# Optimization experiments

Hardware: AMD Instinct MI355X
Metric: run time of the kernel (lower is better)

Reference implementation:

```python
import jax, jax.numpy as jnp
import numpy as np

N_NODES = 100000
N_EDGES = 1280000
D_IN = 64
D_HID = 128
D_OUT = 64


def sage_conv(x, src, dst, W_l, b_l, W_r, n_nodes):
    # PyG SAGEConv (aggr='mean', root_weight=True):
    #   out_i = W_l @ mean_{j in N(i)} x_j + b_l + W_r @ x_i
    msg = x[src]  # [E, d] gather of source-node features
    agg = jax.ops.segment_sum(msg, dst, num_segments=n_nodes)  # [N, d]
    cnt = jax.ops.segment_sum(jnp.ones((src.shape[0], 1), x.dtype), dst,
                              num_segments=n_nodes)  # [N, 1]
    mean = agg / jnp.maximum(cnt, 1.0)  # zero-neighbor nodes -> 0 (matches scatter-mean)
    return mean @ W_l.T + b_l + x @ W_r.T


def setup_inputs() -> dict:
    key = jax.random.key(0)
    ks = jax.random.split(key, 8)
    x = jax.random.normal(ks[0], (N_NODES, D_IN), dtype=jnp.float32)
    edge_index = jax.random.randint(ks[1], (2, N_EDGES), 0, N_NODES, dtype=jnp.int64)
    s = 0.05
    W_l1 = jax.random.normal(ks[2], (D_HID, D_IN), dtype=jnp.float32) * s
    b_l1 = jnp.zeros((D_HID,), dtype=jnp.float32)
    W_r1 = jax.random.normal(ks[3], (D_HID, D_IN), dtype=jnp.float32) * s
    W_l2 = jax.random.normal(ks[4], (D_OUT, D_HID), dtype=jnp.float32) * s
    b_l2 = jnp.zeros((D_OUT,), dtype=jnp.float32)
    W_r2 = jax.random.normal(ks[5], (D_OUT, D_HID), dtype=jnp.float32) * s
    return {"x": x, "edge_index": edge_index,
            "W_l1": W_l1, "b_l1": b_l1, "W_r1": W_r1,
            "W_l2": W_l2, "b_l2": b_l2, "W_r2": W_r2}


def reference(x, edge_index, W_l1, b_l1, W_r1, W_l2, b_l2, W_r2):
    src, dst = edge_index[0], edge_index[1]
    n = x.shape[0]
    h = sage_conv(x, src, dst, W_l1, b_l1, W_r1, n)
    h = jax.nn.relu(h)
    out = sage_conv(h, src, dst, W_l2, b_l2, W_r2, n)
    return out
```

## Files before the change

### kernel.cpp

```cpp
#include <hip/hip_runtime.h>
#include <cstdint>
#include <cstddef>

typedef __attribute__((ext_vector_type(8))) short short8;
typedef __attribute__((ext_vector_type(4))) float floatx4;
typedef __attribute__((ext_vector_type(2))) float floatx2;
typedef __attribute__((ext_vector_type(4))) int intx4;

static constexpr int DIN  = 64;
static constexpr int DHID = 128;
static constexpr int BSH  = 7;
static constexpr int BNODES = 1 << BSH;
static constexpr int TILE = 8192;
static constexpr int CAP  = 4096;
static constexpr unsigned SENT = 0xFFFFFFFFu;

__device__ inline short f2bf(float f) {
  unsigned u = __float_as_uint(f);
  u += 0x7FFF + ((u >> 16) & 1);
  return (short)(u >> 16);
}
__device__ inline float bf2f(short s) {
  return __uint_as_float(((unsigned)(unsigned short)s) << 16);
}
__device__ inline floatx2 bfpair(unsigned u) {
  floatx2 r;
  r[0] = __uint_as_float(u << 16);
  r[1] = __uint_as_float(u & 0xFFFF0000u);
  return r;
}

__global__ __launch_bounds__(256) void part_prep_kernel(const void* edges, long long nmax,
    int* __restrict__ bucket_cursor, int* __restrict__ real_cnt,
    unsigned* __restrict__ packed, int E, int NB,
    const float* __restrict__ x,
    const float* __restrict__ Wl1, const float* __restrict__ Wr1,
    const float* __restrict__ Wl2, const float* __restrict__ Wr2,
    short* __restrict__ xb, short* __restrict__ wc1, short* __restrict__ wc2,
    int nx, int gP, int gx)
{
  __shared__ unsigned sval[TILE];
  __shared__ unsigned saux[TILE];
  __shared__ int hist[1024];
  __shared__ int gb[1024];
  __shared__ int smode;
  int t = threadIdx.x;
  int blk = blockIdx.x;
  if (blk >= gP) {
    int b = blk - gP;
    if (b < gx) {
      int i0 = (b * 256 + t) * 8;
      if (i0 < nx) {
        floatx4 f0 = *(const floatx4*)&x[i0];
        floatx4 f1 = *(const floatx4*)&x[i0 + 4];
        short8 o;
        o[0]=f2bf(f0[0]); o[1]=f2bf(f0[1]); o[2]=f2bf(f0[2]); o[3]=f2bf(f0[3]);
        o[4]=f2bf(f1[0]); o[5]=f2bf(f1[1]); o[6]=f2bf(f1[2]); o[7]=f2bf(f1[3]);
        *(short8*)&xb[i0] = o;
      }
    } else {
      int wb = b - gx;
      int idx = ((wb & 15) * 256 + t) * 4;
      int n = idx >> 7, k = idx & 127;
      const float* src;
      if (wb < 16) src = (k < 64) ? &Wl1[n * 64 + k] : &Wr1[n * 64 + (k - 64)];
      else         src = (n < 64) ? &Wl2[n * 128 + k] : &Wr2[(n - 64) * 128 + k];
      floatx4 f = *(const floatx4*)src;
      short* dst = (wb < 16 ? wc1 : wc2) + idx;
      dst[0]=f2bf(f[0]); dst[1]=f2bf(f[1]); dst[2]=f2bf(f[2]); dst[3]=f2bf(f[3]);
    }
    return;
  }
  int base = blk * TILE;
  int cnt_here = E - base; if (cnt_here > TILE) cnt_here = TILE;
  for (int i = t; i < NB; i += 256) hist[i] = 0;
  if (t == 0) smode = 1;
  __syncthreads();
  {
    const long long* e64 = (const long long*)edges;
    int nchk = E < 256 ? E : 256;
    bool ok = true;
    for (int i = t; i < nchk; i += 256) {
      long long v = e64[i];
      if (v < 0 || v >= nmax) ok = false;
    }
    if (!ok) smode = 0;
  }
  __syncthreads();
  bool m64 = (smode != 0);
  #pragma unroll 4
  for (int c = 0; c < TILE / 256; ++c) {
    int idx = c * 256 + t;
    if (idx < cnt_here) {
      int i = base + idx;
      int s, d;
      if (m64) { const long long* e = (const long long*)edges; s = (int)e[i]; d = (int)e[(size_t)E + i]; }
      else     { const int*       e = (const int*)edges;       s = e[i];      d = e[(size_t)E + i]; }
      int b = d >> BSH;
      int rank = atomicAdd(&hist[b], 1);
      sval[idx] = ((unsigned)(d & (BNODES - 1)) << 17) | (unsigned)s;
      saux[idx] = ((unsigned)b << 13) | (unsigned)rank;
    }
  }
  __syncthreads();
  for (int b = t; b < NB; b += 256) {
    int cnt = hist[b];
    int gbase = 0;
    if (cnt > 0) {
      int pad = (cnt + 15) & ~15;
      gbase = b * CAP + atomicAdd(&bucket_cursor[b], pad);
      atomicAdd(&real_cnt[b], cnt);
      for (int j = cnt; j < pad; ++j) packed[gbase + j] = SENT;
    }
    gb[b] = gbase;
  }
  __syncthreads();
  #pragma unroll 4
  for (int c = 0; c < TILE / 256; ++c) {
    int idx = c * 256 + t;
    if (idx < cnt_here) {
      unsigned a = saux[idx];
      packed[gb[a >> 13] + (a & 0x1FFFu)] = sval[idx];
    }
  }
}

__global__ __launch_bounds__(256) void bucket_sort_kernel(const unsigned* __restrict__ packed,
                                                          const int* __restrict__ bucket_cursor,
                                                          const int* __restrict__ real_cnt,
                                                          int* __restrict__ row_ptr,
                                                          int* __restrict__ sorted_src, int N, int E) {
  __shared__ int nhist[BNODES];
  __shared__ int cur[BNODES];
  __shared__ int wsum[4];
  __shared__ int redsum[4];
  int b = blockIdx.x, t = threadIdx.x;
  int partial = 0;
  for (int i = t; i < b; i += 256) partial += real_cnt[i];
  #pragma unroll
  for (int off = 1; off < 64; off <<= 1) partial += __shfl_xor(partial, off, 64);
  if ((t & 63) == 0) redsum[t >> 6] = partial;
  if (t < BNODES) nhist[t] = 0;
  if (b == 0 && t == 0) row_ptr[N] = E;
  __syncthreads();
  int eb = redsum[0] + redsum[1] + redsum[2] + redsum[3];
  int n0 = b << BSH;
  int nn = N - n0; if (nn > BNODES) nn = BNODES;
  int rbeg = b * CAP, rcnt = bucket_cursor[b];
  for (int i = t; i < rcnt; i += 256) {
    unsigned p = packed[rbeg + i];
    if (p != SENT) atomicAdd(&nhist[p >> 17], 1);
  }
  __syncthreads();
  int lane = t & 63, w = t >> 6;
  int v = (t < BNODES) ? nhist[t] : 0;
  int val = v;
  #pragma unroll
  for (int off = 1; off < 64; off <<= 1) {
    int u = __shfl_up(val, off, 64);
    if (lane >= off) val += u;
  }
  if (lane == 63) wsum[w] = val;
  __syncthreads();
  int pre = (w == 1) ? wsum[0] : 0;
  int excl = pre + val - v;
  if (t < nn) { row_ptr[n0 + t] = eb + excl; cur[t] = eb + excl; }
  __syncthreads();
  for (int i = t; i < rcnt; i += 256) {
    unsigned p = packed[rbeg + i];
    if (p != SENT) {
      int pos = atomicAdd(&cur[p >> 17], 1);
      sorted_src[pos] = (int)(p & 0x1FFFFu);
    }
  }
}

template <bool EPI>
__global__ __launch_bounds__(256) void agg_bf16_kernel(const short* __restrict__ feat,
                                                       const int* __restrict__ row_ptr,
                                                       const int* __restrict__ srcs,
                                                       const float* __restrict__ rbuf,
                                                       const float* __restrict__ bias,
                                                       short* __restrict__ outb,
                                                       float* __restrict__ outf, int N) {
  int node = blockIdx.x * 32 + (threadIdx.x >> 3);
  if (node >= N) return;
  int c = threadIdx.x & 7;
  const short* fbase = feat + c * 8;
  int beg = row_ptr[node], end = row_ptr[node + 1];
  floatx2 acc2[4];
  #pragma unroll
  for (int k = 0; k < 4; ++k) acc2[k] = (floatx2){0.f, 0.f};
  int e = beg;
  for (; e + 8 <= end; e += 8) {
    intx4 sa = *(const intx4*)&srcs[e];
    intx4 sb = *(const intx4*)&srcs[e + 4];
    short8 v0 = *(const short8*)&fbase[(size_t)sa[0] * 64];
    short8 v1 = *(const short8*)&fbase[(size_t)sa[1] * 64];
    short8 v2 = *(const short8*)&fbase[(size_t)sa[2] * 64];
    short8 v3 = *(const short8*)&fbase[(size_t)sa[3] * 64];
    short8 v4 = *(const short8*)&fbase[(size_t)sb[0] * 64];
    short8 v5 = *(const short8*)&fbase[(size_t)sb[1] * 64];
    short8 v6 = *(const short8*)&fbase[(size_t)sb[2] * 64];
    short8 v7 = *(const short8*)&fbase[(size_t)sb[3] * 64];
    const unsigned* u0 = (const unsigned*)&v0;
    const unsigned* u1 = (const unsigned*)&v1;
    const unsigned* u2 = (const unsigned*)&v2;
    const unsigned* u3 = (const unsigned*)&v3;
    const unsigned* u4 = (const unsigned*)&v4;
    const unsigned* u5 = (const unsigned*)&v5;
    const unsigned* u6 = (const unsigned*)&v6;
    const unsigned* u7 = (const unsigned*)&v7;
    #pragma unroll
    for (int k = 0; k < 4; ++k) {
      floatx2 s01 = bfpair(u0[k]) + bfpair(u1[k]);
      floatx2 s23 = bfpair(u2[k]) + bfpair(u3[k]);
      floatx2 s45 = bfpair(u4[k]) + bfpair(u5[k]);
      floatx2 s67 = bfpair(u6[k]) + bfpair(u7[k]);
      acc2[k] += (s01 + s23) + (s45 + s67);
    }
  }
  for (; e + 4 <= end; e += 4) {
    intx4 sa = *(const intx4*)&srcs[e];
    short8 v0 = *(const short8*)&fbase[(size_t)sa[0] * 64];
    short8 v1 = *(const short8*)&fbase[(size_t)sa[1] * 64];
    short8 v2 = *(const short8*)&fbase[(size_t)sa[2] * 64];
    short8 v3 = *(const short8*)&fbase[(size_t)sa[3] * 64];
    const unsigned* u0 = (const unsigned*)&v0;
    const unsigned* u1 = (const unsigned*)&v1;
    const unsigned* u2 = (const unsigned*)&v2;
    const unsigned* u3 = (const unsigned*)&v3;
    #pragma unroll
    for (int k = 0; k < 4; ++k) {
      floatx2 s01 = bfpair(u0[k]) + bfpair(u1[k]);
      floatx2 s23 = bfpair(u2[k]) + bfpair(u3[k]);
      acc2[k] += s01 + s23;
    }
  }
  for (; e < end; ++e) {
    short8 v = *(const short8*)&fbase[(size_t)srcs[e] * 64];
    const unsigned* u = (const unsigned*)&v;
    #pragma unroll
    for (int k = 0; k < 4; ++k) acc2[k] += bfpair(u[k]);
  }
  float acc[8];
  #pragma unroll
  for (int k = 0; k < 4; ++k) { acc[2 * k] = acc2[k][0]; acc[2 * k + 1] = acc2[k][1]; }
  float inv = 1.f / fmaxf((float)(end - beg), 1.f);
  if (!EPI) {
    short8 o;
    #pragma unroll
    for (int j = 0; j < 8; ++j) o[j] = f2bf(acc[j] * inv);
    *(short8*)&outb[(size_t)node * 64 + c * 8] = o;
  } else {
    floatx4 b0 = *(const floatx4*)&bias[c * 8];
    floatx4 b1 = *(const floatx4*)&bias[c * 8 + 4];
    floatx4 r0 = *(const floatx4*)&rbuf[(size_t)node * 64 + c * 8];
    floatx4 r1 = *(const floatx4*)&rbuf[(size_t)node * 64 + c * 8 + 4];
    floatx4 o0, o1;
    #pragma unroll
    for (int j = 0; j < 4; ++j) {
      o0[j] = acc[j] * inv + b0[j] + r0[j];
      o1[j] = acc[4 + j] * inv + b1[j] + r1[j];
    }
    *(floatx4*)&outf[(size_t)node * 64 + c * 8]     = o0;
    *(floatx4*)&outf[(size_t)node * 64 + c * 8 + 4] = o1;
  }
}

__global__ __launch_bounds__(256) void fused_gemm_kernel(
    const short* __restrict__ Aa, const short* __restrict__ Ab,
    const short* __restrict__ wc1, const short* __restrict__ wc2,
    const float* __restrict__ bias1,
    short* __restrict__ Cg, float* __restrict__ Cr, int M)
{
  __shared__ short Ws[128][136];
  __shared__ short Hs[64][136];
  int t = threadIdx.x;
  #pragma unroll
  for (int i = 0; i < 8; ++i) {
    int idx = i * 256 + t;
    int r = idx >> 4, c8 = (idx & 15) * 8;
    *(short8*)&Ws[r][c8] = *(const short8*)&wc1[r * 128 + c8];
  }
  __syncthreads();
  int wv = t >> 6, lane = t & 63, q = lane >> 4, l15 = lane & 15;
  int m0 = blockIdx.x * 64 + wv * 16;
  int row = m0 + l15;
  bool rowok = row < M;
  floatx4 acc[8];
  #pragma unroll
  for (int nt = 0; nt < 8; ++nt) acc[nt] = (floatx4){0.f, 0.f, 0.f, 0.f};
  #pragma unroll
  for (int ko = 0; ko < 4; ++ko) {
    const short* Asrc = (ko < 2) ? Aa : Ab;
    short8 a = {0, 0, 0, 0, 0, 0, 0, 0};
    if (rowok) a = *(const short8*)&Asrc[(size_t)row * 64 + (ko & 1) * 32 + q * 8];
    #pragma unroll
    for (int nt = 0; nt < 8; ++nt) {
      short8 b = *(const short8*)&Ws[nt * 16 + l15][ko * 32 + q * 8];
      acc[nt] = __builtin_amdgcn_mfma_f32_16x16x32_bf16(a, b, acc[nt], 0, 0, 0);
    }
  }
  #pragma unroll
  for (int nt = 0; nt < 8; ++nt) {
    int n = nt * 16 + l15;
    float bv = bias1[n];
    #pragma unroll
    for (int r2 = 0; r2 < 4; ++r2) {
      int lr = wv * 16 + q * 4 + r2;
      float v = fmaxf(acc[nt][r2] + bv, 0.f);
      Hs[lr][n] = f2bf(v);
    }
  }
  __syncthreads();
  #pragma unroll
  for (int i = 0; i < 8; ++i) {
    int idx = i * 256 + t;
    int r = idx >> 4, c8 = (idx & 15) * 8;
    *(short8*)&Ws[r][c8] = *(const short8*)&wc2[r * 128 + c8];
  }
  __syncthreads();
  #pragma unroll
  for (int nt = 0; nt < 8; ++nt) acc[nt] = (floatx4){0.f, 0.f, 0.f, 0.f};
  #pragma unroll
  for (int ko = 0; ko < 4; ++ko) {
    short8 a = *(const short8*)&Hs[wv * 16 + l15][ko * 32 + q * 8];
    #pragma unroll
    for (int nt = 0; nt < 8; ++nt) {
      short8 b = *(const short8*)&Ws[nt * 16 + l15][ko * 32 + q * 8];
      acc[nt] = __builtin_amdgcn_mfma_f32_16x16x32_bf16(a, b, acc[nt], 0, 0, 0);
    }
  }
  #pragma unroll
  for (int nt = 0; nt < 8; ++nt) {
    int n = nt * 16 + l15;
    #pragma unroll
    for (int r2 = 0; r2 < 4; ++r2) {
      int mr = m0 + q * 4 + r2;
      if (mr >= M) continue;
      float v = acc[nt][r2];
      if (nt < 4) Cg[(size_t)mr * 64 + n] = f2bf(v);
      else        Cr[(size_t)mr * 64 + (n - 64)] = v;
    }
  }
}

extern "C" void kernel_launch(void* const* d_in, const int* in_sizes, int n_in,
                              void* d_out, int out_size, void* d_ws, size_t ws_size,
                              hipStream_t stream) {
  const float* x   = (const float*)d_in[0];
  const void*  ei  = d_in[1];
  const float* Wl1 = (const float*)d_in[2];
  const float* bl1 = (const float*)d_in[3];
  const float* Wr1 = (const float*)d_in[4];
  const float* Wl2 = (const float*)d_in[5];
  const float* bl2 = (const float*)d_in[6];
  const float* Wr2 = (const float*)d_in[7];
  int N = in_sizes[0] / DIN;
  int E = in_sizes[1] / 2;
  int NB = (N + BNODES - 1) / BNODES;

  char* w = (char*)d_ws;
  size_t off = 0;
  auto alloc = [&](size_t bytes) -> void* {
    void* p = w + off;
    off += (bytes + 255) & ~(size_t)255;
    return p;
  };
  int*      bcur       = (int*)alloc((size_t)NB * 8);
  int*      rcnt       = bcur + NB;
  int*      row_ptr    = (int*)alloc(((size_t)N + 1) * 4);
  unsigned* packed     = (unsigned*)alloc((size_t)NB * CAP * 4);
  int*      sorted_src = (int*)alloc((size_t)E * 4);
  short*    xb         = (short*)alloc((size_t)N * 64 * 2);
  short*    meanb      = (short*)alloc((size_t)N * 64 * 2);
  float*    rbuf       = (float*)alloc((size_t)N * 64 * 4);
  short*    wc1        = (short*)alloc(128 * 128 * 2);
  short*    wc2        = (short*)alloc(128 * 128 * 2);
  (void)ws_size; (void)n_in; (void)out_size;

  hipMemsetAsync(bcur, 0, (size_t)NB * 8, stream);

  int nx = N * DIN;
  int gx = (nx / 8 + 255) / 256;
  int gP = (E + TILE - 1) / TILE;
  part_prep_kernel<<<gP + gx + 32, 256, 0, stream>>>(ei, (long long)N, bcur, rcnt, packed,
                                                     E, NB, x, Wl1, Wr1, Wl2, Wr2,
                                                     xb, wc1, wc2, nx, gP, gx);

  bucket_sort_kernel<<<NB, 256, 0, stream>>>(packed, bcur, rcnt, row_ptr, sorted_src, N, E);

  int gN32 = (N + 31) / 32;
  agg_bf16_kernel<false><<<gN32, 256, 0, stream>>>(xb, row_ptr, sorted_src, nullptr, nullptr, meanb, nullptr, N);

  int gm = (N + 63) / 64;
  fused_gemm_kernel<<<gm, 256, 0, stream>>>(meanb, xb, wc1, wc2, bl1, meanb, rbuf, N);

  agg_bf16_kernel<true><<<gN32, 256, 0, stream>>>(meanb, row_ptr, sorted_src, rbuf, bl2, nullptr, (float*)d_out, N);
}
```

Baseline: 203.5 us.

## Replace two-level bucket sort with global-atomic CSR build; widen GEMM tile to 128 rows

Replaces the LDS-partitioned bucket sort (partition kernel plus per-bucket sort kernel) with a classic counting sort: a global atomic degree histogram, a single-block 1024-thread scan, and a scatter pass that uses global atomics on per-node cursors. Separately, the fused GEMM now processes 128 rows per block, with two M-subtiles per wave sharing each B fragment, to improve weight reuse. The new CSR path depends on contended global atomics and on a single-workgroup serial scan over 100k nodes, and it gives up the locality of the bucketed scatter, so it may be slower. The GEMM change doubles accumulator registers and LDS use.

```diff
diff --git a/kernel.cpp b/kernel.cpp
--- a/kernel.cpp
+++ b/kernel.cpp
@@ -9,11 +9,7 @@
 
 static constexpr int DIN  = 64;
 static constexpr int DHID = 128;
-static constexpr int BSH  = 7;
-static constexpr int BNODES = 1 << BSH;
-static constexpr int TILE = 8192;
-static constexpr int CAP  = 4096;
-static constexpr unsigned SENT = 0xFFFFFFFFu;
+static constexpr int HTILE = 2048;
 
 __device__ inline short f2bf(float f) {
   unsigned u = __float_as_uint(f);
@@ -30,24 +26,19 @@
   return r;
 }
 
-__global__ __launch_bounds__(256) void part_prep_kernel(const void* edges, long long nmax,
-    int* __restrict__ bucket_cursor, int* __restrict__ real_cnt,
-    unsigned* __restrict__ packed, int E, int NB,
+__global__ __launch_bounds__(256) void prep_hist_kernel(const void* edges, long long nmax,
+    int* __restrict__ deg, int E,
     const float* __restrict__ x,
     const float* __restrict__ Wl1, const float* __restrict__ Wr1,
     const float* __restrict__ Wl2, const float* __restrict__ Wr2,
     short* __restrict__ xb, short* __restrict__ wc1, short* __restrict__ wc2,
-    int nx, int gP, int gx)
+    int nx, int gH, int gx)
 {
-  __shared__ unsigned sval[TILE];
-  __shared__ unsigned saux[TILE];
-  __shared__ int hist[1024];
-  __shared__ int gb[1024];
   __shared__ int smode;
   int t = threadIdx.x;
   int blk = blockIdx.x;
-  if (blk >= gP) {
-    int b = blk - gP;
+  if (blk >= gH) {
+    int b = blk - gH;
     if (b < gx) {
       int i0 = (b * 256 + t) * 8;
       if (i0 < nx) {
@@ -71,9 +62,6 @@
     }
     return;
   }
-  int base = blk * TILE;
-  int cnt_here = E - base; if (cnt_here > TILE) cnt_here = TILE;
-  for (int i = t; i < NB; i += 256) hist[i] = 0;
   if (t == 0) smode = 1;
   __syncthreads();
   {
@@ -88,89 +76,82 @@
   }
   __syncthreads();
   bool m64 = (smode != 0);
-  #pragma unroll 4
-  for (int c = 0; c < TILE / 256; ++c) {
+  int base = blk * HTILE;
+  int cnt_here = E - base; if (cnt_here > HTILE) cnt_here = HTILE;
+  #pragma unroll
+  for (int c = 0; c < HTILE / 256; ++c) {
+    int idx = c * 256 + t;
+    if (idx < cnt_here) {
+      int i = base + idx;
+      int d;
+      if (m64) { const long long* e = (const long long*)edges; d = (int)e[(size_t)E + i]; }
+      else     { const int*       e = (const int*)edges;       d = e[(size_t)E + i]; }
+      atomicAdd(&deg[d], 1);
+    }
+  }
+}
+
+__global__ __launch_bounds__(1024) void scan_kernel(const int* __restrict__ deg,
+                                                    int* __restrict__ row_ptr,
+                                                    int* __restrict__ cur, int N, int E) {
+  __shared__ int wsums[16];
+  int t = threadIdx.x;
+  int per = (N + 1023) / 1024;
+  int i0 = t * per;
+  int i1 = i0 + per; if (i1 > N) i1 = N;
+  int s = 0;
+  for (int i = i0; i < i1; ++i) s += deg[i];
+  int lane = t & 63, w = t >> 6;
+  int val = s;
+  #pragma unroll
+  for (int off = 1; off < 64; off <<= 1) {
+    int u = __shfl_up(val, off, 64);
+    if (lane >= off) val += u;
+  }
+  if (lane == 63) wsums[w] = val;
+  __syncthreads();
+  int wpre = 0;
+  for (int ww = 0; ww < w; ++ww) wpre += wsums[ww];
+  int run = wpre + val - s;
+  for (int i = i0; i < i1; ++i) {
+    row_ptr[i] = run;
+    cur[i] = run;
+    run += deg[i];
+  }
+  if (t == 0) row_ptr[N] = E;
+}
+
+__global__ __launch_bounds__(256) void scatter_kernel(const void* edges, long long nmax,
+                                                      int* __restrict__ cur,
+                                                      int* __restrict__ sorted_src, int E) {
+  __shared__ int smode;
+  int t = threadIdx.x;
+  if (t == 0) smode = 1;
+  __syncthreads();
+  {
+    const long long* e64 = (const long long*)edges;
+    int nchk = E < 256 ? E : 256;
+    bool ok = true;
+    for (int i = t; i < nchk; i += 256) {
+      long long v = e64[i];
+      if (v < 0 || v >= nmax) ok = false;
+    }
+    if (!ok) smode = 0;
+  }
+  __syncthreads();
+  bool m64 = (smode != 0);
+  int base = blockIdx.x * HTILE;
+  int cnt_here = E - base; if (cnt_here > HTILE) cnt_here = HTILE;
+  #pragma unroll
+  for (int c = 0; c < HTILE / 256; ++c) {
     int idx = c * 256 + t;
     if (idx < cnt_here) {
       int i = base + idx;
       int s, d;
       if (m64) { const long long* e = (const long long*)edges; s = (int)e[i]; d = (int)e[(size_t)E + i]; }
       else     { const int*       e = (const int*)edges;       s = e[i];      d = e[(size_t)E + i]; }
-      int b = d >> BSH;
-      int rank = atomicAdd(&hist[b], 1);
-      sval[idx] = ((unsigned)(d & (BNODES - 1)) << 17) | (unsigned)s;
-      saux[idx] = ((unsigned)b << 13) | (unsigned)rank;
-    }
-  }
-  __syncthreads();
-  for (int b = t; b < NB; b += 256) {
-    int cnt = hist[b];
-    int gbase = 0;
-    if (cnt > 0) {
-      int pad = (cnt + 15) & ~15;
-      gbase = b * CAP + atomicAdd(&bucket_cursor[b], pad);
-      atomicAdd(&real_cnt[b], cnt);
-      for (int j = cnt; j < pad; ++j) packed[gbase + j] = SENT;
-    }
-    gb[b] = gbase;
-  }
-  __syncthreads();
-  #pragma unroll 4
-  for (int c = 0; c < TILE / 256; ++c) {
-    int idx = c * 256 + t;
-    if (idx < cnt_here) {
-      unsigned a = saux[idx];
-      packed[gb[a >> 13] + (a & 0x1FFFu)] = sval[idx];
-    }
-  }
-}
-
-__global__ __launch_bounds__(256) void bucket_sort_kernel(const unsigned* __restrict__ packed,
-                                                          const int* __restrict__ bucket_cursor,
-                                                          const int* __restrict__ real_cnt,
-                                                          int* __restrict__ row_ptr,
-                                                          int* __restrict__ sorted_src, int N, int E) {
-  __shared__ int nhist[BNODES];
-  __shared__ int cur[BNODES];
-  __shared__ int wsum[4];
-  __shared__ int redsum[4];
-  int b = blockIdx.x, t = threadIdx.x;
-  int partial = 0;
-  for (int i = t; i < b; i += 256) partial += real_cnt[i];
-  #pragma unroll
-  for (int off = 1; off < 64; off <<= 1) partial += __shfl_xor(partial, off, 64);
-  if ((t & 63) == 0) redsum[t >> 6] = partial;
-  if (t < BNODES) nhist[t] = 0;
-  if (b == 0 && t == 0) row_ptr[N] = E;
-  __syncthreads();
-  int eb = redsum[0] + redsum[1] + redsum[2] + redsum[3];
-  int n0 = b << BSH;
-  int nn = N - n0; if (nn > BNODES) nn = BNODES;
-  int rbeg = b * CAP, rcnt = bucket_cursor[b];
-  for (int i = t; i < rcnt; i += 256) {
-    unsigned p = packed[rbeg + i];
-    if (p != SENT) atomicAdd(&nhist[p >> 17], 1);
-  }
-  __syncthreads();
-  int lane = t & 63, w = t >> 6;
-  int v = (t < BNODES) ? nhist[t] : 0;
-  int val = v;
-  #pragma unroll
-  for (int off = 1; off < 64; off <<= 1) {
-    int u = __shfl_up(val, off, 64);
-    if (lane >= off) val += u;
-  }
-  if (lane == 63) wsum[w] = val;
-  __syncthreads();
-  int pre = (w == 1) ? wsum[0] : 0;
-  int excl = pre + val - v;
-  if (t < nn) { row_ptr[n0 + t] = eb + excl; cur[t] = eb + excl; }
-  __syncthreads();
-  for (int i = t; i < rcnt; i += 256) {
-    unsigned p = packed[rbeg + i];
-    if (p != SENT) {
-      int pos = atomicAdd(&cur[p >> 17], 1);
-      sorted_src[pos] = (int)(p & 0x1FFFFu);
+      int pos = atomicAdd(&cur[d], 1);
+      sorted_src[pos] = s;
     }
   }
 }
@@ -275,7 +256,7 @@
     short* __restrict__ Cg, float* __restrict__ Cr, int M)
 {
   __shared__ short Ws[128][136];
-  __shared__ short Hs[64][136];
+  __shared__ short Hs[128][136];
   int t = threadIdx.x;
   #pragma unroll
   for (int i = 0; i < 8; ++i) {
@@ -285,32 +266,41 @@
   }
   __syncthreads();
   int wv = t >> 6, lane = t & 63, q = lane >> 4, l15 = lane & 15;
-  int m0 = blockIdx.x * 64 + wv * 16;
-  int row = m0 + l15;
-  bool rowok = row < M;
-  floatx4 acc[8];
-  #pragma unroll
-  for (int nt = 0; nt < 8; ++nt) acc[nt] = (floatx4){0.f, 0.f, 0.f, 0.f};
+  int m0 = blockIdx.x * 128 + wv * 32;
+  floatx4 acc[2][8];
+  #pragma unroll
+  for (int mt = 0; mt < 2; ++mt)
+    #pragma unroll
+    for (int nt = 0; nt < 8; ++nt) acc[mt][nt] = (floatx4){0.f, 0.f, 0.f, 0.f};
   #pragma unroll
   for (int ko = 0; ko < 4; ++ko) {
     const short* Asrc = (ko < 2) ? Aa : Ab;
-    short8 a = {0, 0, 0, 0, 0, 0, 0, 0};
-    if (rowok) a = *(const short8*)&Asrc[(size_t)row * 64 + (ko & 1) * 32 + q * 8];
+    short8 a[2];
+    #pragma unroll
+    for (int mt = 0; mt < 2; ++mt) {
+      int row = m0 + mt * 16 + l15;
+      a[mt] = (short8){0, 0, 0, 0, 0, 0, 0, 0};
+      if (row < M) a[mt] = *(const short8*)&Asrc[(size_t)row * 64 + (ko & 1) * 32 + q * 8];
+    }
     #pragma unroll
     for (int nt = 0; nt < 8; ++nt) {
-      short8 b = *(const short8*)&Ws[nt * 16 + l15][ko * 32 + q * 8];
-      acc[nt] = __builtin_amdgcn_mfma_f32_16x16x32_bf16(a, b, acc[nt], 0, 0, 0);
-    }
-  }
-  #pragma unroll
-  for (int nt = 0; nt < 8; ++nt) {
-    int n = nt * 16 + l15;
-    float bv = bias1[n];
-    #pragma unroll
-    for (int r2 = 0; r2 < 4; ++r2) {
-      int lr = wv * 16 + q * 4 + r2;
-      float v = fmaxf(acc[nt][r2] + bv, 0.f);
-      Hs[lr][n] = f2bf(v);
+      short8 bfr = *(const short8*)&Ws[nt * 16 + l15][ko * 32 + q * 8];
+      acc[0][nt] = __builtin_amdgcn_mfma_f32_16x16x32_bf16(a[0], bfr, acc[0][nt], 0, 0, 0);
+      acc[1][nt] = __builtin_amdgcn_mfma_f32_16x16x32_bf16(a[1], bfr, acc[1][nt], 0, 0, 0);
+    }
+  }
+  #pragma unroll
+  for (int mt = 0; mt < 2; ++mt) {
+    #pragma unroll
+    for (int nt = 0; nt < 8; ++nt) {
+      int n = nt * 16 + l15;
+      float bv = bias1[n];
+      #pragma unroll
+      for (int r2 = 0; r2 < 4; ++r2) {
+        int lr = wv * 32 + mt * 16 + q * 4 + r2;
+        float v = fmaxf(acc[mt][nt][r2] + bv, 0.f);
+        Hs[lr][n] = f2bf(v);
+      }
     }
   }
   __syncthreads();
@@ -322,26 +312,35 @@
   }
   __syncthreads();
   #pragma unroll
-  for (int nt = 0; nt < 8; ++nt) acc[nt] = (floatx4){0.f, 0.f, 0.f, 0.f};
+  for (int mt = 0; mt < 2; ++mt)
+    #pragma unroll
+    for (int nt = 0; nt < 8; ++nt) acc[mt][nt] = (floatx4){0.f, 0.f, 0.f, 0.f};
   #pragma unroll
   for (int ko = 0; ko < 4; ++ko) {
-    short8 a = *(const short8*)&Hs[wv * 16 + l15][ko * 32 + q * 8];
+    short8 a[2];
+    #pragma unroll
+    for (int mt = 0; mt < 2; ++mt)
+      a[mt] = *(const short8*)&Hs[wv * 32 + mt * 16 + l15][ko * 32 + q * 8];
     #pragma unroll
     for (int nt = 0; nt < 8; ++nt) {
-      short8 b = *(const short8*)&Ws[nt * 16 + l15][ko * 32 + q * 8];
-      acc[nt] = __builtin_amdgcn_mfma_f32_16x16x32_bf16(a, b, acc[nt], 0, 0, 0);
-    }
-  }
-  #pragma unroll
-  for (int nt = 0; nt < 8; ++nt) {
-    int n = nt * 16 + l15;
-    #pragma unroll
-    for (int r2 = 0; r2 < 4; ++r2) {
-      int mr = m0 + q * 4 + r2;
-      if (mr >= M) continue;
-      float v = acc[nt][r2];
-      if (nt < 4) Cg[(size_t)mr * 64 + n] = f2bf(v);
-      else        Cr[(size_t)mr * 64 + (n - 64)] = v;
+      short8 bfr = *(const short8*)&Ws[nt * 16 + l15][ko * 32 + q * 8];
+      acc[0][nt] = __builtin_amdgcn_mfma_f32_16x16x32_bf16(a[0], bfr, acc[0][nt], 0, 0, 0);
+      acc[1][nt] = __builtin_amdgcn_mfma_f32_16x16x32_bf16(a[1], bfr, acc[1][nt], 0, 0, 0);
+    }
+  }
+  #pragma unroll
+  for (int mt = 0; mt < 2; ++mt) {
+    #pragma unroll
+    for (int nt = 0; nt < 8; ++nt) {
+      int n = nt * 16 + l15;
+      #pragma unroll
+      for (int r2 = 0; r2 < 4; ++r2) {
+        int mr = m0 + mt * 16 + q * 4 + r2;
+        if (mr >= M) continue;
+        float v = acc[mt][nt][r2];
+        if (nt < 4) Cg[(size_t)mr * 64 + n] = f2bf(v);
+        else        Cr[(size_t)mr * 64 + (n - 64)] = v;
+      }
     }
   }
 }
@@ -359,7 +358,6 @@
   const float* Wr2 = (const float*)d_in[7];
   int N = in_sizes[0] / DIN;
   int E = in_sizes[1] / 2;
-  int NB = (N + BNODES - 1) / BNODES;
 
   char* w = (char*)d_ws;
   size_t off = 0;
@@ -368,10 +366,9 @@
     off += (bytes + 255) & ~(size_t)255;
     return p;
   };
-  int*      bcur       = (int*)alloc((size_t)NB * 8);
-  int*      rcnt       = bcur + NB;
+  int*      deg        = (int*)alloc((size_t)N * 4);
+  int*      cur        = (int*)alloc((size_t)N * 4);
   int*      row_ptr    = (int*)alloc(((size_t)N + 1) * 4);
-  unsigned* packed     = (unsigned*)alloc((size_t)NB * CAP * 4);
   int*      sorted_src = (int*)alloc((size_t)E * 4);
   short*    xb         = (short*)alloc((size_t)N * 64 * 2);
   short*    meanb      = (short*)alloc((size_t)N * 64 * 2);
@@ -380,21 +377,23 @@
   short*    wc2        = (short*)alloc(128 * 128 * 2);
   (void)ws_size; (void)n_in; (void)out_size;
 
-  hipMemsetAsync(bcur, 0, (size_t)NB * 8, stream);
+  hipMemsetAsync(deg, 0, (size_t)N * 4, stream);
 
   int nx = N * DIN;
   int gx = (nx / 8 + 255) / 256;
-  int gP = (E + TILE - 1) / TILE;
-  part_prep_kernel<<<gP + gx + 32, 256, 0, stream>>>(ei, (long long)N, bcur, rcnt, packed,
-                                                     E, NB, x, Wl1, Wr1, Wl2, Wr2,
-                                                     xb, wc1, wc2, nx, gP, gx);
-
-  bucket_sort_kernel<<<NB, 256, 0, stream>>>(packed, bcur, rcnt, row_ptr, sorted_src, N, E);
+  int gH = (E + HTILE - 1) / HTILE;
+  prep_hist_kernel<<<gH + gx + 32, 256, 0, stream>>>(ei, (long long)N, deg, E,
+                                                     x, Wl1, Wr1, Wl2, Wr2,
+                                                     xb, wc1, wc2, nx, gH, gx);
+
+  scan_kernel<<<1, 1024, 0, stream>>>(deg, row_ptr, cur, N, E);
+
+  scatter_kernel<<<gH, 256, 0, stream>>>(ei, (long long)N, cur, sorted_src, E);
 
   int gN32 = (N + 31) / 32;
   agg_bf16_kernel<false><<<gN32, 256, 0, stream>>>(xb, row_ptr, sorted_src, nullptr, nullptr, meanb, nullptr, N);
 
-  int gm = (N + 63) / 64;
+  int gm = (N + 127) / 128;
   fused_gemm_kernel<<<gm, 256, 0, stream>>>(meanb, xb, wc1, wc2, bl1, meanb, rbuf, N);
 
   agg_bf16_kernel<true><<<gN32, 256, 0, stream>>>(meanb, row_ptr, sorted_src, rbuf, bl2, nullptr, (float*)d_out, N);
```

Measured after the change: 539.5 us. 2.65x slower.
